# Kernel optimization log

Measured on AMD Instinct MI355X. Metric: run time of the kernel, lower is better.

## Reference

```python
import jax, jax.numpy as jnp
import numpy as np

N = 20000      # nodes
E = 320000     # edges (before self-loops)
C_IN, C_HID, C_OUT = 256, 256, 128
NEG_SLOPE = 0.2  # PyG GATConv default


def setup_inputs() -> dict:
    key = jax.random.key(0)
    ks = jax.random.split(key, 10)
    x = jax.random.normal(ks[0], (N, C_IN), dtype=jnp.float32)
    edge_index = jax.random.randint(ks[1], (2, E), 0, N, dtype=jnp.int64)

    def glorot(k, shape, fan):
        return jax.random.normal(k, shape, dtype=jnp.float32) / np.float32(np.sqrt(fan))

    W1 = glorot(ks[2], (C_IN, C_HID), C_IN)
    a_src1 = glorot(ks[3], (C_HID,), C_HID)
    a_dst1 = glorot(ks[4], (C_HID,), C_HID)
    b1 = jnp.zeros((C_HID,), jnp.float32)
    W2 = glorot(ks[5], (C_HID, C_OUT), C_HID)
    a_src2 = glorot(ks[6], (C_OUT,), C_OUT)
    a_dst2 = glorot(ks[7], (C_OUT,), C_OUT)
    b2 = jnp.zeros((C_OUT,), jnp.float32)
    return dict(x=x, edge_index=edge_index, W1=W1, a_src1=a_src1, a_dst1=a_dst1,
                b1=b1, W2=W2, a_src2=a_src2, a_dst2=a_dst2, b2=b2)


def gat_layer(x, src, dst, W, a_src, a_dst, b, n):
    # PyG GATConv (heads=1): linear proj, additive attention, softmax over
    # incoming edges per destination node, weighted aggregation + bias.
    h = x @ W                                   # [N, F]
    alpha_src = h @ a_src                       # [N]
    alpha_dst = h @ a_dst                       # [N]
    e = jax.nn.leaky_relu(alpha_src[src] + alpha_dst[dst], NEG_SLOPE)  # [E]
    m = jax.ops.segment_max(e, dst, num_segments=n)                    # stable softmax
    e = jnp.exp(e - m[dst])
    denom = jax.ops.segment_sum(e, dst, num_segments=n)                # [N]
    out = jax.ops.segment_sum(e[:, None] * h[src], dst, num_segments=n)  # [N, F]
    return out / denom[:, None] + b


def reference(x, edge_index, W1, a_src1, a_dst1, b1, W2, a_src2, a_dst2, b2):
    n = x.shape[0]
    # GATConv adds self-loops by default
    loops = jnp.arange(n, dtype=edge_index.dtype)
    ei = jnp.concatenate([edge_index, jnp.stack([loops, loops])], axis=1)
    src, dst = ei[0], ei[1]
    h = gat_layer(x, src, dst, W1, a_src1, a_dst1, b1, n)
    h = jax.nn.relu(h)  # Dropout is identity in eval mode
    return gat_layer(h, src, dst, W2, a_src2, a_dst2, b2, n)
```

## Files before the change

kernel.cpp:

```cpp
#include <hip/hip_runtime.h>
#include <math.h>

#define N_NODES 20000
#define N_EDGES 320000
#define C_IN  256
#define C_HID 256
#define C_OUT 128
#define NEG_SLOPE 0.2f
#define CAP   256
#define GEMM1_BLKS (N_NODES / 32)
#define SCAT_BLKS  ((N_EDGES + 255) / 256)
#define AGG_PAD 280

typedef __attribute__((ext_vector_type(8))) short bf16x8;
typedef __attribute__((ext_vector_type(4))) float f32x4;

__device__ __align__(16) unsigned short c_W1h[C_IN * C_HID], c_W1l[C_IN * C_HID];
__device__ __align__(16) unsigned short c_W2h[C_HID * C_OUT], c_W2l[C_HID * C_OUT];
__device__ float c_as1f[C_HID], c_ad1f[C_HID], c_b1f[C_HID];
__device__ float c_as2f[C_OUT], c_ad2f[C_OUT], c_b2f[C_OUT];
__device__ __align__(16) unsigned short g_h1b[(size_t)N_NODES * C_HID];
__device__ __align__(16) unsigned short g_h2b[(size_t)N_NODES * C_OUT];
__device__ float g_alps1[N_NODES], g_alpd1[N_NODES];
__device__ float g_alps2[N_NODES], g_alpd2[N_NODES];
__device__ int   g_cursor[N_NODES];
__device__ int   g_srcidx[(size_t)N_NODES * CAP];
__device__ int   g_is64;
__device__ int   g_isf32;

__device__ __forceinline__ float bf2f(unsigned short b){
  unsigned int u = ((unsigned int)b) << 16;
  return __builtin_bit_cast(float, u);
}
__device__ __forceinline__ unsigned short f2bf(float f){
  unsigned int u = __builtin_bit_cast(unsigned int, f);
  u += 0x7fffu + ((u >> 16) & 1u);
  return (unsigned short)(u >> 16);
}
__device__ __forceinline__ int clampi(int v){
  v = v < 0 ? 0 : v;
  return v >= N_NODES ? N_NODES - 1 : v;
}
__device__ __forceinline__ void edge_sd(const int* ei, int e, int& s, int& d){
  if (g_is64){ s = ei[2 * e]; d = ei[2 * (N_EDGES + e)]; }
  else       { s = ei[e];     d = ei[N_EDGES + e]; }
  s = clampi(s); d = clampi(d);
}

struct Ptrs { const void* p[8]; };

__device__ __forceinline__ int wpack(int k, int n, int Nc){
  return (((k >> 5) * (Nc / 16) + (n >> 4)) * 64 + (((k >> 3) & 3) * 16 + (n & 15))) * 8 + (k & 7);
}

#define PREP_Z  N_NODES
#define PREP_W1 (C_IN * C_HID)
#define PREP_W2 (C_HID * C_OUT)
#define PREP_T  (PREP_Z + PREP_W1 + PREP_W2 + 2 * C_HID + C_HID + 2 * C_OUT + C_OUT)

__global__ void prep_k(const unsigned int* __restrict__ xw,
                       const int* __restrict__ ei, Ptrs ps){
  __shared__ int s_isf32;
  if (threadIdx.x < 64){
    int lane = (int)threadIdx.x, cnt = 0;
    for (int j = lane; j < 256; j += 64){
      unsigned int e = (xw[j] >> 7) & 0xFFu;
      if (e >= 0x60u && e <= 0x8Fu) ++cnt;
    }
#pragma unroll
    for (int o = 32; o > 0; o >>= 1) cnt += __shfl_xor(cnt, o, 64);
    if (lane == 0) s_isf32 = (cnt < 200) ? 1 : 0;
  }
  __syncthreads();
  const int isf32 = s_isf32;

  if (blockIdx.x == 0 && threadIdx.x < 64){
    unsigned long long anybad = __ballot(ei[2 * (int)threadIdx.x + 1] != 0);
    if (threadIdx.x == 0){ g_isf32 = isf32; g_is64 = (anybad == 0ULL) ? 1 : 0; }
  }

  int tid = (int)(blockIdx.x * blockDim.x + threadIdx.x);
  if (tid < PREP_Z){
    g_cursor[tid] = 0;
    return;
  }
  int j = tid - PREP_Z;
  auto ld = [&](const void* p, int i) -> float {
    return isf32 ? ((const float*)p)[i] : bf2f(((const unsigned short*)p)[i]);
  };
  if (j < PREP_W1){
    float f = ld(ps.p[0], j);
    int k = j / C_HID, n = j % C_HID;
    int idx = wpack(k, n, C_HID);
    unsigned short h = f2bf(f);
    c_W1h[idx] = h; c_W1l[idx] = f2bf(f - bf2f(h));
    return;
  }
  j -= PREP_W1;
  if (j < PREP_W2){
    float f = ld(ps.p[4], j);
    int k = j / C_OUT, n = j % C_OUT;
    int idx = wpack(k, n, C_OUT);
    unsigned short h = f2bf(f);
    c_W2h[idx] = h; c_W2l[idx] = f2bf(f - bf2f(h));
    return;
  }
  j -= PREP_W2;
  if      (j <  256) c_as1f[j]        = ld(ps.p[1], j);
  else if (j <  512) c_ad1f[j - 256]  = ld(ps.p[2], j - 256);
  else if (j <  768) c_b1f [j - 512]  = ld(ps.p[3], j - 512);
  else if (j <  896) c_as2f[j - 768]  = ld(ps.p[5], j - 768);
  else if (j < 1024) c_ad2f[j - 896]  = ld(ps.p[6], j - 896);
  else if (j < 1152) c_b2f [j - 1024] = ld(ps.p[7], j - 1024);
}

__global__ __launch_bounds__(256) void gemm1_k(const void* __restrict__ xsrc,
                                               const int* __restrict__ ei){
  if (blockIdx.x >= GEMM1_BLKS){
    int e = (int)(blockIdx.x - GEMM1_BLKS) * 256 + (int)threadIdx.x;
    if (e < N_EDGES){
      int s, d;
      edge_sd(ei, e, s, d);
      int pos = atomicAdd(&g_cursor[d], 1);
      if (pos < CAP) g_srcidx[(size_t)d * CAP + pos] = s;
    }
    return;
  }

  __shared__ float s_ps[4][32], s_pd[4][32];

  const bool isf32 = (g_isf32 != 0);
  int wid  = (int)(threadIdx.x >> 6);
  int lane = (int)(threadIdx.x & 63);
  int kgrp = lane >> 4, cl = lane & 15;
  int mbase = blockIdx.x * 32;

  f32x4 acc[2][4];
#pragma unroll
  for (int m = 0; m < 2; ++m)
#pragma unroll
    for (int n = 0; n < 4; ++n) acc[m][n] = (f32x4){0.f, 0.f, 0.f, 0.f};

  for (int kt = 0; kt < 8; ++kt){
    int kbase = kt * 32 + kgrp * 8;
    bf16x8 ah[2], al[2];
    if (isf32){
      const float* Xf = (const float*)xsrc;
#pragma unroll
      for (int m = 0; m < 2; ++m){
        const float4* xp = (const float4*)(Xf + (size_t)(mbase + m * 16 + cl) * 256 + kbase);
        float4 v0 = xp[0], v1 = xp[1];
        float vals[8] = {v0.x, v0.y, v0.z, v0.w, v1.x, v1.y, v1.z, v1.w};
#pragma unroll
        for (int j = 0; j < 8; ++j){
          unsigned short h = f2bf(vals[j]);
          ah[m][j] = (short)h;
          al[m][j] = (short)f2bf(vals[j] - bf2f(h));
        }
      }
    } else {
      const unsigned short* Xb = (const unsigned short*)xsrc;
#pragma unroll
      for (int m = 0; m < 2; ++m){
        ah[m] = *(const bf16x8*)(Xb + (size_t)(mbase + m * 16 + cl) * 256 + kbase);
        al[m] = (bf16x8){0,0,0,0,0,0,0,0};
      }
    }
#pragma unroll
    for (int nn = 0; nn < 4; ++nn){
      int nt = wid * 4 + nn;
      size_t wi = ((size_t)(kt * 16 + nt) * 64 + lane) * 8;
      bf16x8 bh = *(const bf16x8*)(c_W1h + wi);
      bf16x8 bl = *(const bf16x8*)(c_W1l + wi);
#pragma unroll
      for (int m = 0; m < 2; ++m){
        acc[m][nn] = __builtin_amdgcn_mfma_f32_16x16x32_bf16(ah[m], bh, acc[m][nn], 0, 0, 0);
        acc[m][nn] = __builtin_amdgcn_mfma_f32_16x16x32_bf16(ah[m], bl, acc[m][nn], 0, 0, 0);
        acc[m][nn] = __builtin_amdgcn_mfma_f32_16x16x32_bf16(al[m], bh, acc[m][nn], 0, 0, 0);
      }
    }
  }

  float asv[4], adv[4];
#pragma unroll
  for (int nn = 0; nn < 4; ++nn){
    int col = (wid * 4 + nn) * 16 + cl;
    asv[nn] = c_as1f[col]; adv[nn] = c_ad1f[col];
  }
#pragma unroll
  for (int m = 0; m < 2; ++m){
#pragma unroll
    for (int i = 0; i < 4; ++i){
      int rl = m * 16 + kgrp * 4 + i;
      int row = mbase + rl;
      float ps = 0.f, pd = 0.f;
#pragma unroll
      for (int nn = 0; nn < 4; ++nn){
        int col = (wid * 4 + nn) * 16 + cl;
        float v = acc[m][nn][i];
        g_h1b[(size_t)row * C_HID + col] = f2bf(v);
        ps += v * asv[nn]; pd += v * adv[nn];
      }
      ps += __shfl_xor(ps, 1);  pd += __shfl_xor(pd, 1);
      ps += __shfl_xor(ps, 2);  pd += __shfl_xor(pd, 2);
      ps += __shfl_xor(ps, 4);  pd += __shfl_xor(pd, 4);
      ps += __shfl_xor(ps, 8);  pd += __shfl_xor(pd, 8);
      if (cl == 0){ s_ps[wid][rl] = ps; s_pd[wid][rl] = pd; }
    }
  }
  __syncthreads();
  if (threadIdx.x < 32){
    int r = (int)threadIdx.x;
    g_alps1[mbase + r] = s_ps[0][r] + s_ps[1][r] + s_ps[2][r] + s_ps[3][r];
    g_alpd1[mbase + r] = s_pd[0][r] + s_pd[1][r] + s_pd[2][r] + s_pd[3][r];
  }
}

#define ACC4(p, ww) { \
  a0 += (ww) * bf2f((unsigned short)((p).x & 0xFFFFu)); \
  a1 += (ww) * bf2f((unsigned short)((p).x >> 16)); \
  a2 += (ww) * bf2f((unsigned short)((p).y & 0xFFFFu)); \
  a3 += (ww) * bf2f((unsigned short)((p).y >> 16)); }

#define ACC2(p, ww) { \
  a0 += (ww) * bf2f((unsigned short)((p) & 0xFFFFu)); \
  a1 += (ww) * bf2f((unsigned short)((p) >> 16)); }

__global__ __launch_bounds__(256) void aggemm_k(){
  __shared__ __align__(16) unsigned short s_hi[16 * AGG_PAD];
  __shared__ __align__(16) unsigned short s_lo[16 * AGG_PAD];
  __shared__ float s_ps[4][16], s_pd[4][16];

  int lane = (int)(threadIdx.x & 63);
  int wid  = (int)(threadIdx.x >> 6);
  int nb   = blockIdx.x * 16;
  const uint2* H2 = (const uint2*)g_h1b;

  for (int q = 0; q < 4; ++q){
    int n = nb + wid * 4 + q;
    int len = g_cursor[n]; if (len > CAP) len = CAP;
    int i0 = n * CAP, i1 = i0 + len;
    float adn = g_alpd1[n];
    float dpart = 0.f;
    float a0 = 0.f, a1 = 0.f, a2 = 0.f, a3 = 0.f;

    {
      float es = g_alps1[n] + adn;
      es = (es > 0.f) ? es : NEG_SLOPE * es;
      float wself = __expf(es);
      if (lane == 0) dpart += wself;
      uint2 p = H2[(size_t)n * 64 + lane];
      ACC4(p, wself)
    }

    for (int base = i0; base < i1; base += 64){
      int nv = i1 - base; if (nv > 64) nv = 64;
      int sv = 0; float wv = 0.f;
      if (lane < nv){
        sv = g_srcidx[base + lane];
        float e = g_alps1[sv] + adn;
        e = (e > 0.f) ? e : NEG_SLOPE * e;
        wv = __expf(e);
      }
      dpart += wv;
      int j = 0;
      for (; j + 8 <= nv; j += 8){
        int s0 = __shfl(sv, j),     s1 = __shfl(sv, j + 1);
        int s2 = __shfl(sv, j + 2), s3 = __shfl(sv, j + 3);
        int s4 = __shfl(sv, j + 4), s5 = __shfl(sv, j + 5);
        int s6 = __shfl(sv, j + 6), s7 = __shfl(sv, j + 7);
        float w0 = __shfl(wv, j),     w1 = __shfl(wv, j + 1);
        float w2 = __shfl(wv, j + 2), w3 = __shfl(wv, j + 3);
        float w4 = __shfl(wv, j + 4), w5 = __shfl(wv, j + 5);
        float w6 = __shfl(wv, j + 6), w7 = __shfl(wv, j + 7);
        uint2 p0 = H2[(size_t)s0 * 64 + lane];
        uint2 p1 = H2[(size_t)s1 * 64 + lane];
        uint2 p2 = H2[(size_t)s2 * 64 + lane];
        uint2 p3 = H2[(size_t)s3 * 64 + lane];
        uint2 p4 = H2[(size_t)s4 * 64 + lane];
        uint2 p5 = H2[(size_t)s5 * 64 + lane];
        uint2 p6 = H2[(size_t)s6 * 64 + lane];
        uint2 p7 = H2[(size_t)s7 * 64 + lane];
        ACC4(p0, w0) ACC4(p1, w1) ACC4(p2, w2) ACC4(p3, w3)
        ACC4(p4, w4) ACC4(p5, w5) ACC4(p6, w6) ACC4(p7, w7)
      }
      for (; j + 4 <= nv; j += 4){
        int s0 = __shfl(sv, j),     s1 = __shfl(sv, j + 1);
        int s2 = __shfl(sv, j + 2), s3 = __shfl(sv, j + 3);
        float w0 = __shfl(wv, j),     w1 = __shfl(wv, j + 1);
        float w2 = __shfl(wv, j + 2), w3 = __shfl(wv, j + 3);
        uint2 p0 = H2[(size_t)s0 * 64 + lane];
        uint2 p1 = H2[(size_t)s1 * 64 + lane];
        uint2 p2 = H2[(size_t)s2 * 64 + lane];
        uint2 p3 = H2[(size_t)s3 * 64 + lane];
        ACC4(p0, w0) ACC4(p1, w1) ACC4(p2, w2) ACC4(p3, w3)
      }
      for (; j < nv; ++j){
        int s = __shfl(sv, j);
        float w = __shfl(wv, j);
        uint2 p = H2[(size_t)s * 64 + lane];
        ACC4(p, w)
      }
    }

    float den = dpart;
#pragma unroll
    for (int o = 32; o > 0; o >>= 1) den += __shfl_xor(den, o, 64);
    float inv = 1.f / den;

    float o0 = a0 * inv + c_b1f[4 * lane];
    float o1 = a1 * inv + c_b1f[4 * lane + 1];
    float o2 = a2 * inv + c_b1f[4 * lane + 2];
    float o3 = a3 * inv + c_b1f[4 * lane + 3];
    o0 = fmaxf(o0, 0.f); o1 = fmaxf(o1, 0.f);
    o2 = fmaxf(o2, 0.f); o3 = fmaxf(o3, 0.f);
    unsigned short h0 = f2bf(o0), h1 = f2bf(o1), h2 = f2bf(o2), h3 = f2bf(o3);
    uint2 ph, pl;
    ph.x = (unsigned)h0 | ((unsigned)h1 << 16);
    ph.y = (unsigned)h2 | ((unsigned)h3 << 16);
    pl.x = (unsigned)f2bf(o0 - bf2f(h0)) | ((unsigned)f2bf(o1 - bf2f(h1)) << 16);
    pl.y = (unsigned)f2bf(o2 - bf2f(h2)) | ((unsigned)f2bf(o3 - bf2f(h3)) << 16);
    int r = wid * 4 + q;
    *(uint2*)&s_hi[r * AGG_PAD + 4 * lane] = ph;
    *(uint2*)&s_lo[r * AGG_PAD + 4 * lane] = pl;
  }
  __syncthreads();

  int kgrp = lane >> 4, cl = lane & 15;
  f32x4 acc[2];
  acc[0] = (f32x4){0.f, 0.f, 0.f, 0.f};
  acc[1] = (f32x4){0.f, 0.f, 0.f, 0.f};
  for (int kt = 0; kt < 8; ++kt){
    int rb = cl * AGG_PAD + kt * 32 + kgrp * 8;
    bf16x8 ah = *(const bf16x8*)&s_hi[rb];
    bf16x8 al = *(const bf16x8*)&s_lo[rb];
#pragma unroll
    for (int nn = 0; nn < 2; ++nn){
      int nt = wid * 2 + nn;
      size_t wi = ((size_t)(kt * 8 + nt) * 64 + lane) * 8;
      bf16x8 bh = *(const bf16x8*)(c_W2h + wi);
      bf16x8 bl = *(const bf16x8*)(c_W2l + wi);
      acc[nn] = __builtin_amdgcn_mfma_f32_16x16x32_bf16(ah, bh, acc[nn], 0, 0, 0);
      acc[nn] = __builtin_amdgcn_mfma_f32_16x16x32_bf16(ah, bl, acc[nn], 0, 0, 0);
      acc[nn] = __builtin_amdgcn_mfma_f32_16x16x32_bf16(al, bh, acc[nn], 0, 0, 0);
    }
  }

  float asv[2], adv[2];
#pragma unroll
  for (int nn = 0; nn < 2; ++nn){
    int col = (wid * 2 + nn) * 16 + cl;
    asv[nn] = c_as2f[col]; adv[nn] = c_ad2f[col];
  }
#pragma unroll
  for (int i = 0; i < 4; ++i){
    int row = nb + kgrp * 4 + i;
    float ps = 0.f, pd = 0.f;
#pragma unroll
    for (int nn = 0; nn < 2; ++nn){
      int col = (wid * 2 + nn) * 16 + cl;
      float v = acc[nn][i];
      g_h2b[(size_t)row * C_OUT + col] = f2bf(v);
      ps += v * asv[nn]; pd += v * adv[nn];
    }
    ps += __shfl_xor(ps, 1);  pd += __shfl_xor(pd, 1);
    ps += __shfl_xor(ps, 2);  pd += __shfl_xor(pd, 2);
    ps += __shfl_xor(ps, 4);  pd += __shfl_xor(pd, 4);
    ps += __shfl_xor(ps, 8);  pd += __shfl_xor(pd, 8);
    if (cl == 0){ s_ps[wid][kgrp * 4 + i] = ps; s_pd[wid][kgrp * 4 + i] = pd; }
  }
  __syncthreads();
  if (threadIdx.x < 16){
    int r = (int)threadIdx.x;
    g_alps2[nb + r] = s_ps[0][r] + s_ps[1][r] + s_ps[2][r] + s_ps[3][r];
    g_alpd2[nb + r] = s_pd[0][r] + s_pd[1][r] + s_pd[2][r] + s_pd[3][r];
  }
}

__global__ __launch_bounds__(256) void agg2_k(float* OUT){
  int lane = (int)(threadIdx.x & 63);
  int n = blockIdx.x * 4 + (int)(threadIdx.x >> 6);
  int len = g_cursor[n]; if (len > CAP) len = CAP;
  int i0 = n * CAP, i1 = i0 + len;
  float adn = g_alpd2[n];
  float dpart = 0.f;
  float a0 = 0.f, a1 = 0.f;
  const unsigned int* H1 = (const unsigned int*)g_h2b;

  {
    float es = g_alps2[n] + adn;
    es = (es > 0.f) ? es : NEG_SLOPE * es;
    float wself = __expf(es);
    if (lane == 0) dpart += wself;
    unsigned int p = H1[(size_t)n * 64 + lane];
    ACC2(p, wself)
  }

  for (int base = i0; base < i1; base += 64){
    int nv = i1 - base; if (nv > 64) nv = 64;
    int sv = 0; float wv = 0.f;
    if (lane < nv){
      sv = g_srcidx[base + lane];
      float e = g_alps2[sv] + adn;
      e = (e > 0.f) ? e : NEG_SLOPE * e;
      wv = __expf(e);
    }
    dpart += wv;
    int j = 0;
    for (; j + 8 <= nv; j += 8){
      int s0 = __shfl(sv, j),     s1 = __shfl(sv, j + 1);
      int s2 = __shfl(sv, j + 2), s3 = __shfl(sv, j + 3);
      int s4 = __shfl(sv, j + 4), s5 = __shfl(sv, j + 5);
      int s6 = __shfl(sv, j + 6), s7 = __shfl(sv, j + 7);
      float w0 = __shfl(wv, j),     w1 = __shfl(wv, j + 1);
      float w2 = __shfl(wv, j + 2), w3 = __shfl(wv, j + 3);
      float w4 = __shfl(wv, j + 4), w5 = __shfl(wv, j + 5);
      float w6 = __shfl(wv, j + 6), w7 = __shfl(wv, j + 7);
      unsigned int p0 = H1[(size_t)s0 * 64 + lane];
      unsigned int p1 = H1[(size_t)s1 * 64 + lane];
      unsigned int p2 = H1[(size_t)s2 * 64 + lane];
      unsigned int p3 = H1[(size_t)s3 * 64 + lane];
      unsigned int p4 = H1[(size_t)s4 * 64 + lane];
      unsigned int p5 = H1[(size_t)s5 * 64 + lane];
      unsigned int p6 = H1[(size_t)s6 * 64 + lane];
      unsigned int p7 = H1[(size_t)s7 * 64 + lane];
      ACC2(p0, w0) ACC2(p1, w1) ACC2(p2, w2) ACC2(p3, w3)
      ACC2(p4, w4) ACC2(p5, w5) ACC2(p6, w6) ACC2(p7, w7)
    }
    for (; j + 4 <= nv; j += 4){
      int s0 = __shfl(sv, j),     s1 = __shfl(sv, j + 1);
      int s2 = __shfl(sv, j + 2), s3 = __shfl(sv, j + 3);
      float w0 = __shfl(wv, j),     w1 = __shfl(wv, j + 1);
      float w2 = __shfl(wv, j + 2), w3 = __shfl(wv, j + 3);
      unsigned int p0 = H1[(size_t)s0 * 64 + lane];
      unsigned int p1 = H1[(size_t)s1 * 64 + lane];
      unsigned int p2 = H1[(size_t)s2 * 64 + lane];
      unsigned int p3 = H1[(size_t)s3 * 64 + lane];
      ACC2(p0, w0) ACC2(p1, w1) ACC2(p2, w2) ACC2(p3, w3)
    }
    for (; j < nv; ++j){
      int s = __shfl(sv, j);
      float w = __shfl(wv, j);
      unsigned int p = H1[(size_t)s * 64 + lane];
      ACC2(p, w)
    }
  }

  float den = dpart;
#pragma unroll
  for (int o = 32; o > 0; o >>= 1) den += __shfl_xor(den, o, 64);
  float inv = 1.f / den;

  float2 o;
  o.x = a0 * inv + c_b2f[2 * lane];
  o.y = a1 * inv + c_b2f[2 * lane + 1];
  ((float2*)OUT)[(size_t)n * 64 + lane] = o;
}

extern "C" void kernel_launch(void* const* d_in, const int* in_sizes, int n_in,
                              void* d_out, int out_size, void* d_ws, size_t ws_size,
                              hipStream_t stream){
  (void)in_sizes; (void)n_in; (void)out_size; (void)d_ws; (void)ws_size;
  const void* x  = d_in[0];
  const int*  ei = (const int*)d_in[1];
  float* out = (float*)d_out;

  Ptrs ps;
  ps.p[0] = d_in[2]; ps.p[1] = d_in[3]; ps.p[2] = d_in[4]; ps.p[3] = d_in[5];
  ps.p[4] = d_in[6]; ps.p[5] = d_in[7]; ps.p[6] = d_in[8]; ps.p[7] = d_in[9];

  prep_k<<<(PREP_T + 255) / 256, 256, 0, stream>>>((const unsigned int*)x, ei, ps);

  gemm1_k<<<GEMM1_BLKS + SCAT_BLKS, 256, 0, stream>>>(x, ei);

  aggemm_k<<<N_NODES / 16, 256, 0, stream>>>();

  agg2_k<<<N_NODES / 4, 256, 0, stream>>>(out);
}
```

Baseline: 164.6 us.

## Fuse all GAT stages into one cooperative persistent kernel with grid syncs

Merges the prep, GEMM1-plus-scatter, aggregate-plus-GEMM2 and final aggregation kernels into a single cooperative kernel. Stages are separated by grid-wide syncs, and within each stage work tiles are handed out through global atomic counters. The aim is to remove the separate kernel launches and the idle tail between stages. In exchange it adds grid-sync cost, one atomic per tile, and occupancy limits from `launch_bounds(256,4)`, with a fallback to the old multi-kernel path if the cooperative launch fails.

```diff
diff --git a/kernel.cpp b/kernel.cpp
--- a/kernel.cpp
+++ b/kernel.cpp
@@ -1,5 +1,8 @@
 #include <hip/hip_runtime.h>
+#include <hip/hip_cooperative_groups.h>
 #include <math.h>
+
+namespace cg = cooperative_groups;
 
 #define N_NODES 20000
 #define N_EDGES 320000
@@ -10,6 +13,8 @@
 #define CAP   256
 #define GEMM1_BLKS (N_NODES / 32)
 #define SCAT_BLKS  ((N_EDGES + 255) / 256)
+#define AGGEMM_BLKS (N_NODES / 16)
+#define AGG2_BLKS  (N_NODES / 4)
 #define AGG_PAD 280
 
 typedef __attribute__((ext_vector_type(8))) short bf16x8;
@@ -27,6 +32,7 @@
 __device__ int   g_srcidx[(size_t)N_NODES * CAP];
 __device__ int   g_is64;
 __device__ int   g_isf32;
+__device__ int   g_q1, g_q2, g_q3;
 
 __device__ __forceinline__ float bf2f(unsigned short b){
   unsigned int u = ((unsigned int)b) << 16;
@@ -41,22 +47,442 @@
   v = v < 0 ? 0 : v;
   return v >= N_NODES ? N_NODES - 1 : v;
 }
+
+struct Ptrs { const void* p[8]; };
+
+__device__ __forceinline__ int wpack(int k, int n, int Nc){
+  return (((k >> 5) * (Nc / 16) + (n >> 4)) * 64 + (((k >> 3) & 3) * 16 + (n & 15))) * 8 + (k & 7);
+}
+
+#define PREP_Z  N_NODES
+#define PREP_W1 (C_IN * C_HID)
+#define PREP_W2 (C_HID * C_OUT)
+#define PREP_T  (PREP_Z + PREP_W1 + PREP_W2 + 2 * C_HID + C_HID + 2 * C_OUT + C_OUT)
+
+#define ACC4(p, ww) { \
+  a0 += (ww) * bf2f((unsigned short)((p).x & 0xFFFFu)); \
+  a1 += (ww) * bf2f((unsigned short)((p).x >> 16)); \
+  a2 += (ww) * bf2f((unsigned short)((p).y & 0xFFFFu)); \
+  a3 += (ww) * bf2f((unsigned short)((p).y >> 16)); }
+
+#define ACC2(p, ww) { \
+  a0 += (ww) * bf2f((unsigned short)((p) & 0xFFFFu)); \
+  a1 += (ww) * bf2f((unsigned short)((p) >> 16)); }
+
+__global__ __launch_bounds__(256, 4) void fused_k(const unsigned int* __restrict__ xw,
+                                                  const int* __restrict__ ei,
+                                                  float* __restrict__ OUT,
+                                                  Ptrs ps){
+  __shared__ __align__(16) unsigned short s_hi[16 * AGG_PAD];
+  __shared__ __align__(16) unsigned short s_lo[16 * AGG_PAD];
+  __shared__ float s_ps[4][32], s_pd[4][32];
+  __shared__ int s_flags, s_vb;
+
+  const int tidx = (int)threadIdx.x;
+  const int lane = tidx & 63;
+  const int wid  = tidx >> 6;
+
+  if (tidx < 64){
+    int cnt = 0;
+    for (int j = lane; j < 256; j += 64){
+      unsigned int e = (xw[j] >> 7) & 0xFFu;
+      if (e >= 0x60u && e <= 0x8Fu) ++cnt;
+    }
+#pragma unroll
+    for (int o = 32; o > 0; o >>= 1) cnt += __shfl_xor(cnt, o, 64);
+    unsigned long long anybad = __ballot(ei[2 * lane + 1] != 0);
+    if (lane == 0) s_flags = ((cnt < 200) ? 1 : 0) | ((anybad == 0ULL) ? 2 : 0);
+  }
+  if (blockIdx.x == 0 && tidx == 0){ g_q1 = 0; g_q2 = 0; g_q3 = 0; }
+  __syncthreads();
+  const bool isf32 = (s_flags & 1) != 0;
+  const bool is64  = (s_flags & 2) != 0;
+
+  const int total = (int)(gridDim.x * blockDim.x);
+  auto ld = [&](const void* p, int i) -> float {
+    return isf32 ? ((const float*)p)[i] : bf2f(((const unsigned short*)p)[i]);
+  };
+  for (int t = (int)(blockIdx.x * blockDim.x) + tidx; t < PREP_T; t += total){
+    if (t < PREP_Z){ g_cursor[t] = 0; continue; }
+    int j = t - PREP_Z;
+    if (j < PREP_W1){
+      float f = ld(ps.p[0], j);
+      int k = j / C_HID, n = j % C_HID;
+      int idx = wpack(k, n, C_HID);
+      unsigned short h = f2bf(f);
+      c_W1h[idx] = h; c_W1l[idx] = f2bf(f - bf2f(h));
+      continue;
+    }
+    j -= PREP_W1;
+    if (j < PREP_W2){
+      float f = ld(ps.p[4], j);
+      int k = j / C_OUT, n = j % C_OUT;
+      int idx = wpack(k, n, C_OUT);
+      unsigned short h = f2bf(f);
+      c_W2h[idx] = h; c_W2l[idx] = f2bf(f - bf2f(h));
+      continue;
+    }
+    j -= PREP_W2;
+    if      (j <  256) c_as1f[j]        = ld(ps.p[1], j);
+    else if (j <  512) c_ad1f[j - 256]  = ld(ps.p[2], j - 256);
+    else if (j <  768) c_b1f [j - 512]  = ld(ps.p[3], j - 512);
+    else if (j <  896) c_as2f[j - 768]  = ld(ps.p[5], j - 768);
+    else if (j < 1024) c_ad2f[j - 896]  = ld(ps.p[6], j - 896);
+    else if (j < 1152) c_b2f [j - 1024] = ld(ps.p[7], j - 1024);
+  }
+
+  __threadfence();
+  cg::this_grid().sync();
+
+  for (;;){
+    __syncthreads();
+    if (tidx == 0) s_vb = atomicAdd(&g_q1, 1);
+    __syncthreads();
+    const int vb = s_vb;
+    if (vb >= GEMM1_BLKS + SCAT_BLKS) break;
+
+    if (vb >= GEMM1_BLKS){
+      int e = (vb - GEMM1_BLKS) * 256 + tidx;
+      if (e < N_EDGES){
+        int s, d;
+        if (is64){ s = ei[2 * e]; d = ei[2 * (N_EDGES + e)]; }
+        else     { s = ei[e];     d = ei[N_EDGES + e]; }
+        s = clampi(s); d = clampi(d);
+        int pos = atomicAdd(&g_cursor[d], 1);
+        if (pos < CAP) g_srcidx[(size_t)d * CAP + pos] = s;
+      }
+      continue;
+    }
+
+    int kgrp = lane >> 4, cl = lane & 15;
+    int mbase = vb * 32;
+    f32x4 acc[2][4];
+#pragma unroll
+    for (int m = 0; m < 2; ++m)
+#pragma unroll
+      for (int n = 0; n < 4; ++n) acc[m][n] = (f32x4){0.f, 0.f, 0.f, 0.f};
+
+    for (int kt = 0; kt < 8; ++kt){
+      int kbase = kt * 32 + kgrp * 8;
+      bf16x8 ah[2], al[2];
+      if (isf32){
+        const float* Xf = (const float*)xw;
+#pragma unroll
+        for (int m = 0; m < 2; ++m){
+          const float4* xp = (const float4*)(Xf + (size_t)(mbase + m * 16 + cl) * 256 + kbase);
+          float4 v0 = xp[0], v1 = xp[1];
+          float vals[8] = {v0.x, v0.y, v0.z, v0.w, v1.x, v1.y, v1.z, v1.w};
+#pragma unroll
+          for (int j = 0; j < 8; ++j){
+            unsigned short h = f2bf(vals[j]);
+            ah[m][j] = (short)h;
+            al[m][j] = (short)f2bf(vals[j] - bf2f(h));
+          }
+        }
+      } else {
+        const unsigned short* Xb = (const unsigned short*)xw;
+#pragma unroll
+        for (int m = 0; m < 2; ++m){
+          ah[m] = *(const bf16x8*)(Xb + (size_t)(mbase + m * 16 + cl) * 256 + kbase);
+          al[m] = (bf16x8){0,0,0,0,0,0,0,0};
+        }
+      }
+#pragma unroll
+      for (int nn = 0; nn < 4; ++nn){
+        int nt = wid * 4 + nn;
+        size_t wi = ((size_t)(kt * 16 + nt) * 64 + lane) * 8;
+        bf16x8 bh = *(const bf16x8*)(c_W1h + wi);
+        bf16x8 bl = *(const bf16x8*)(c_W1l + wi);
+#pragma unroll
+        for (int m = 0; m < 2; ++m){
+          acc[m][nn] = __builtin_amdgcn_mfma_f32_16x16x32_bf16(ah[m], bh, acc[m][nn], 0, 0, 0);
+          acc[m][nn] = __builtin_amdgcn_mfma_f32_16x16x32_bf16(ah[m], bl, acc[m][nn], 0, 0, 0);
+          acc[m][nn] = __builtin_amdgcn_mfma_f32_16x16x32_bf16(al[m], bh, acc[m][nn], 0, 0, 0);
+        }
+      }
+    }
+
+    float asv[4], adv[4];
+#pragma unroll
+    for (int nn = 0; nn < 4; ++nn){
+      int col = (wid * 4 + nn) * 16 + cl;
+      asv[nn] = c_as1f[col]; adv[nn] = c_ad1f[col];
+    }
+#pragma unroll
+    for (int m = 0; m < 2; ++m){
+#pragma unroll
+      for (int i = 0; i < 4; ++i){
+        int rl = m * 16 + kgrp * 4 + i;
+        int row = mbase + rl;
+        float psum = 0.f, pdum = 0.f;
+#pragma unroll
+        for (int nn = 0; nn < 4; ++nn){
+          int col = (wid * 4 + nn) * 16 + cl;
+          float v = acc[m][nn][i];
+          g_h1b[(size_t)row * C_HID + col] = f2bf(v);
+          psum += v * asv[nn]; pdum += v * adv[nn];
+        }
+        psum += __shfl_xor(psum, 1);  pdum += __shfl_xor(pdum, 1);
+        psum += __shfl_xor(psum, 2);  pdum += __shfl_xor(pdum, 2);
+        psum += __shfl_xor(psum, 4);  pdum += __shfl_xor(pdum, 4);
+        psum += __shfl_xor(psum, 8);  pdum += __shfl_xor(pdum, 8);
+        if (cl == 0){ s_ps[wid][rl] = psum; s_pd[wid][rl] = pdum; }
+      }
+    }
+    __syncthreads();
+    if (tidx < 32){
+      int r = tidx;
+      g_alps1[mbase + r] = s_ps[0][r] + s_ps[1][r] + s_ps[2][r] + s_ps[3][r];
+      g_alpd1[mbase + r] = s_pd[0][r] + s_pd[1][r] + s_pd[2][r] + s_pd[3][r];
+    }
+  }
+
+  __threadfence();
+  cg::this_grid().sync();
+
+  for (;;){
+    __syncthreads();
+    if (tidx == 0) s_vb = atomicAdd(&g_q2, 1);
+    __syncthreads();
+    const int vb = s_vb;
+    if (vb >= AGGEMM_BLKS) break;
+    const int nb = vb * 16;
+    const uint2* H2 = (const uint2*)g_h1b;
+
+    for (int q = 0; q < 4; ++q){
+      int n = nb + wid * 4 + q;
+      int len = g_cursor[n]; if (len > CAP) len = CAP;
+      int i0 = n * CAP, i1 = i0 + len;
+      float adn = g_alpd1[n];
+      float dpart = 0.f;
+      float a0 = 0.f, a1 = 0.f, a2 = 0.f, a3 = 0.f;
+
+      {
+        float es = g_alps1[n] + adn;
+        es = (es > 0.f) ? es : NEG_SLOPE * es;
+        float wself = __expf(es);
+        if (lane == 0) dpart += wself;
+        uint2 p = H2[(size_t)n * 64 + lane];
+        ACC4(p, wself)
+      }
+
+      for (int base = i0; base < i1; base += 64){
+        int nv = i1 - base; if (nv > 64) nv = 64;
+        int sv = 0; float wv = 0.f;
+        if (lane < nv){
+          sv = g_srcidx[base + lane];
+          float e = g_alps1[sv] + adn;
+          e = (e > 0.f) ? e : NEG_SLOPE * e;
+          wv = __expf(e);
+        }
+        dpart += wv;
+        int j = 0;
+        for (; j + 8 <= nv; j += 8){
+          int t0 = __shfl(sv, j),     t1 = __shfl(sv, j + 1);
+          int t2 = __shfl(sv, j + 2), t3 = __shfl(sv, j + 3);
+          int t4 = __shfl(sv, j + 4), t5 = __shfl(sv, j + 5);
+          int t6 = __shfl(sv, j + 6), t7 = __shfl(sv, j + 7);
+          float w0 = __shfl(wv, j),     w1 = __shfl(wv, j + 1);
+          float w2 = __shfl(wv, j + 2), w3 = __shfl(wv, j + 3);
+          float w4 = __shfl(wv, j + 4), w5 = __shfl(wv, j + 5);
+          float w6 = __shfl(wv, j + 6), w7 = __shfl(wv, j + 7);
+          uint2 p0 = H2[(size_t)t0 * 64 + lane];
+          uint2 p1 = H2[(size_t)t1 * 64 + lane];
+          uint2 p2 = H2[(size_t)t2 * 64 + lane];
+          uint2 p3 = H2[(size_t)t3 * 64 + lane];
+          uint2 p4 = H2[(size_t)t4 * 64 + lane];
+          uint2 p5 = H2[(size_t)t5 * 64 + lane];
+          uint2 p6 = H2[(size_t)t6 * 64 + lane];
+          uint2 p7 = H2[(size_t)t7 * 64 + lane];
+          ACC4(p0, w0) ACC4(p1, w1) ACC4(p2, w2) ACC4(p3, w3)
+          ACC4(p4, w4) ACC4(p5, w5) ACC4(p6, w6) ACC4(p7, w7)
+        }
+        for (; j + 4 <= nv; j += 4){
+          int t0 = __shfl(sv, j),     t1 = __shfl(sv, j + 1);
+          int t2 = __shfl(sv, j + 2), t3 = __shfl(sv, j + 3);
+          float w0 = __shfl(wv, j),     w1 = __shfl(wv, j + 1);
+          float w2 = __shfl(wv, j + 2), w3 = __shfl(wv, j + 3);
+          uint2 p0 = H2[(size_t)t0 * 64 + lane];
+          uint2 p1 = H2[(size_t)t1 * 64 + lane];
+          uint2 p2 = H2[(size_t)t2 * 64 + lane];
+          uint2 p3 = H2[(size_t)t3 * 64 + lane];
+          ACC4(p0, w0) ACC4(p1, w1) ACC4(p2, w2) ACC4(p3, w3)
+        }
+        for (; j < nv; ++j){
+          int t = __shfl(sv, j);
+          float w = __shfl(wv, j);
+          uint2 p = H2[(size_t)t * 64 + lane];
+          ACC4(p, w)
+        }
+      }
+
+      float den = dpart;
+#pragma unroll
+      for (int o = 32; o > 0; o >>= 1) den += __shfl_xor(den, o, 64);
+      float inv = 1.f / den;
+
+      float o0 = a0 * inv + c_b1f[4 * lane];
+      float o1 = a1 * inv + c_b1f[4 * lane + 1];
+      float o2 = a2 * inv + c_b1f[4 * lane + 2];
+      float o3 = a3 * inv + c_b1f[4 * lane + 3];
+      o0 = fmaxf(o0, 0.f); o1 = fmaxf(o1, 0.f);
+      o2 = fmaxf(o2, 0.f); o3 = fmaxf(o3, 0.f);
+      unsigned short h0 = f2bf(o0), h1 = f2bf(o1), h2 = f2bf(o2), h3 = f2bf(o3);
+      uint2 ph, pl;
+      ph.x = (unsigned)h0 | ((unsigned)h1 << 16);
+      ph.y = (unsigned)h2 | ((unsigned)h3 << 16);
+      pl.x = (unsigned)f2bf(o0 - bf2f(h0)) | ((unsigned)f2bf(o1 - bf2f(h1)) << 16);
+      pl.y = (unsigned)f2bf(o2 - bf2f(h2)) | ((unsigned)f2bf(o3 - bf2f(h3)) << 16);
+      int r = wid * 4 + q;
+      *(uint2*)&s_hi[r * AGG_PAD + 4 * lane] = ph;
+      *(uint2*)&s_lo[r * AGG_PAD + 4 * lane] = pl;
+    }
+    __syncthreads();
+
+    int kgrp = lane >> 4, cl = lane & 15;
+    f32x4 acc2[2];
+    acc2[0] = (f32x4){0.f, 0.f, 0.f, 0.f};
+    acc2[1] = (f32x4){0.f, 0.f, 0.f, 0.f};
+    for (int kt = 0; kt < 8; ++kt){
+      int rb = cl * AGG_PAD + kt * 32 + kgrp * 8;
+      bf16x8 ah = *(const bf16x8*)&s_hi[rb];
+      bf16x8 al = *(const bf16x8*)&s_lo[rb];
+#pragma unroll
+      for (int nn = 0; nn < 2; ++nn){
+        int nt = wid * 2 + nn;
+        size_t wi = ((size_t)(kt * 8 + nt) * 64 + lane) * 8;
+        bf16x8 bh = *(const bf16x8*)(c_W2h + wi);
+        bf16x8 bl = *(const bf16x8*)(c_W2l + wi);
+        acc2[nn] = __builtin_amdgcn_mfma_f32_16x16x32_bf16(ah, bh, acc2[nn], 0, 0, 0);
+        acc2[nn] = __builtin_amdgcn_mfma_f32_16x16x32_bf16(ah, bl, acc2[nn], 0, 0, 0);
+        acc2[nn] = __builtin_amdgcn_mfma_f32_16x16x32_bf16(al, bh, acc2[nn], 0, 0, 0);
+      }
+    }
+
+    float asv[2], adv[2];
+#pragma unroll
+    for (int nn = 0; nn < 2; ++nn){
+      int col = (wid * 2 + nn) * 16 + cl;
+      asv[nn] = c_as2f[col]; adv[nn] = c_ad2f[col];
+    }
+#pragma unroll
+    for (int i = 0; i < 4; ++i){
+      int row = nb + kgrp * 4 + i;
+      float psum = 0.f, pdum = 0.f;
+#pragma unroll
+      for (int nn = 0; nn < 2; ++nn){
+        int col = (wid * 2 + nn) * 16 + cl;
+        float v = acc2[nn][i];
+        g_h2b[(size_t)row * C_OUT + col] = f2bf(v);
+        psum += v * asv[nn]; pdum += v * adv[nn];
+      }
+      psum += __shfl_xor(psum, 1);  pdum += __shfl_xor(pdum, 1);
+      psum += __shfl_xor(psum, 2);  pdum += __shfl_xor(pdum, 2);
+      psum += __shfl_xor(psum, 4);  pdum += __shfl_xor(pdum, 4);
+      psum += __shfl_xor(psum, 8);  pdum += __shfl_xor(pdum, 8);
+      if (cl == 0){ s_ps[wid][kgrp * 4 + i] = psum; s_pd[wid][kgrp * 4 + i] = pdum; }
+    }
+    __syncthreads();
+    if (tidx < 16){
+      int r = tidx;
+      g_alps2[nb + r] = s_ps[0][r] + s_ps[1][r] + s_ps[2][r] + s_ps[3][r];
+      g_alpd2[nb + r] = s_pd[0][r] + s_pd[1][r] + s_pd[2][r] + s_pd[3][r];
+    }
+  }
+
+  __threadfence();
+  cg::this_grid().sync();
+
+  const unsigned int* H1 = (const unsigned int*)g_h2b;
+  for (;;){
+    __syncthreads();
+    if (tidx == 0) s_vb = atomicAdd(&g_q3, 1);
+    __syncthreads();
+    const int vb = s_vb;
+    if (vb >= AGG2_BLKS) break;
+    int n = vb * 4 + wid;
+    int len = g_cursor[n]; if (len > CAP) len = CAP;
+    int i0 = n * CAP, i1 = i0 + len;
+    float adn = g_alpd2[n];
+    float dpart = 0.f;
+    float a0 = 0.f, a1 = 0.f;
+
+    {
+      float es = g_alps2[n] + adn;
+      es = (es > 0.f) ? es : NEG_SLOPE * es;
+      float wself = __expf(es);
+      if (lane == 0) dpart += wself;
+      unsigned int p = H1[(size_t)n * 64 + lane];
+      ACC2(p, wself)
+    }
+
+    for (int base = i0; base < i1; base += 64){
+      int nv = i1 - base; if (nv > 64) nv = 64;
+      int sv = 0; float wv = 0.f;
+      if (lane < nv){
+        sv = g_srcidx[base + lane];
+        float e = g_alps2[sv] + adn;
+        e = (e > 0.f) ? e : NEG_SLOPE * e;
+        wv = __expf(e);
+      }
+      dpart += wv;
+      int j = 0;
+      for (; j + 8 <= nv; j += 8){
+        int t0 = __shfl(sv, j),     t1 = __shfl(sv, j + 1);
+        int t2 = __shfl(sv, j + 2), t3 = __shfl(sv, j + 3);
+        int t4 = __shfl(sv, j + 4), t5 = __shfl(sv, j + 5);
+        int t6 = __shfl(sv, j + 6), t7 = __shfl(sv, j + 7);
+        float w0 = __shfl(wv, j),     w1 = __shfl(wv, j + 1);
+        float w2 = __shfl(wv, j + 2), w3 = __shfl(wv, j + 3);
+        float w4 = __shfl(wv, j + 4), w5 = __shfl(wv, j + 5);
+        float w6 = __shfl(wv, j + 6), w7 = __shfl(wv, j + 7);
+        unsigned int p0 = H1[(size_t)t0 * 64 + lane];
+        unsigned int p1 = H1[(size_t)t1 * 64 + lane];
+        unsigned int p2 = H1[(size_t)t2 * 64 + lane];
+        unsigned int p3 = H1[(size_t)t3 * 64 + lane];
+        unsigned int p4 = H1[(size_t)t4 * 64 + lane];
+        unsigned int p5 = H1[(size_t)t5 * 64 + lane];
+        unsigned int p6 = H1[(size_t)t6 * 64 + lane];
+        unsigned int p7 = H1[(size_t)t7 * 64 + lane];
+        ACC2(p0, w0) ACC2(p1, w1) ACC2(p2, w2) ACC2(p3, w3)
+        ACC2(p4, w4) ACC2(p5, w5) ACC2(p6, w6) ACC2(p7, w7)
+      }
+      for (; j + 4 <= nv; j += 4){
+        int t0 = __shfl(sv, j),     t1 = __shfl(sv, j + 1);
+        int t2 = __shfl(sv, j + 2), t3 = __shfl(sv, j + 3);
+        float w0 = __shfl(wv, j),     w1 = __shfl(wv, j + 1);
+        float w2 = __shfl(wv, j + 2), w3 = __shfl(wv, j + 3);
+        unsigned int p0 = H1[(size_t)t0 * 64 + lane];
+        unsigned int p1 = H1[(size_t)t1 * 64 + lane];
+        unsigned int p2 = H1[(size_t)t2 * 64 + lane];
+        unsigned int p3 = H1[(size_t)t3 * 64 + lane];
+        ACC2(p0, w0) ACC2(p1, w1) ACC2(p2, w2) ACC2(p3, w3)
+      }
+      for (; j < nv; ++j){
+        int t = __shfl(sv, j);
+        float w = __shfl(wv, j);
+        unsigned int p = H1[(size_t)t * 64 + lane];
+        ACC2(p, w)
+      }
+    }
+
+    float den = dpart;
+#pragma unroll
+    for (int o = 32; o > 0; o >>= 1) den += __shfl_xor(den, o, 64);
+    float inv = 1.f / den;
+
+    float2 o;
+    o.x = a0 * inv + c_b2f[2 * lane];
+    o.y = a1 * inv + c_b2f[2 * lane + 1];
+    ((float2*)OUT)[(size_t)n * 64 + lane] = o;
+  }
+}
+
 __device__ __forceinline__ void edge_sd(const int* ei, int e, int& s, int& d){
   if (g_is64){ s = ei[2 * e]; d = ei[2 * (N_EDGES + e)]; }
   else       { s = ei[e];     d = ei[N_EDGES + e]; }
   s = clampi(s); d = clampi(d);
 }
-
-struct Ptrs { const void* p[8]; };
-
-__device__ __forceinline__ int wpack(int k, int n, int Nc){
-  return (((k >> 5) * (Nc / 16) + (n >> 4)) * 64 + (((k >> 3) & 3) * 16 + (n & 15))) * 8 + (k & 7);
-}
-
-#define PREP_Z  N_NODES
-#define PREP_W1 (C_IN * C_HID)
-#define PREP_W2 (C_HID * C_OUT)
-#define PREP_T  (PREP_Z + PREP_W1 + PREP_W2 + 2 * C_HID + C_HID + 2 * C_OUT + C_OUT)
 
 __global__ void prep_k(const unsigned int* __restrict__ xw,
                        const int* __restrict__ ei, Ptrs ps){
@@ -80,10 +506,7 @@
   }
 
   int tid = (int)(blockIdx.x * blockDim.x + threadIdx.x);
-  if (tid < PREP_Z){
-    g_cursor[tid] = 0;
-    return;
-  }
+  if (tid < PREP_Z){ g_cursor[tid] = 0; return; }
   int j = tid - PREP_Z;
   auto ld = [&](const void* p, int i) -> float {
     return isf32 ? ((const float*)p)[i] : bf2f(((const unsigned short*)p)[i]);
@@ -128,7 +551,6 @@
   }
 
   __shared__ float s_ps[4][32], s_pd[4][32];
-
   const bool isf32 = (g_isf32 != 0);
   int wid  = (int)(threadIdx.x >> 6);
   int lane = (int)(threadIdx.x & 63);
@@ -215,16 +637,6 @@
     g_alpd1[mbase + r] = s_pd[0][r] + s_pd[1][r] + s_pd[2][r] + s_pd[3][r];
   }
 }
-
-#define ACC4(p, ww) { \
-  a0 += (ww) * bf2f((unsigned short)((p).x & 0xFFFFu)); \
-  a1 += (ww) * bf2f((unsigned short)((p).x >> 16)); \
-  a2 += (ww) * bf2f((unsigned short)((p).y & 0xFFFFu)); \
-  a3 += (ww) * bf2f((unsigned short)((p).y >> 16)); }
-
-#define ACC2(p, ww) { \
-  a0 += (ww) * bf2f((unsigned short)((p) & 0xFFFFu)); \
-  a1 += (ww) * bf2f((unsigned short)((p) >> 16)); }
 
 __global__ __launch_bounds__(256) void aggemm_k(){
   __shared__ __align__(16) unsigned short s_hi[16 * AGG_PAD];
@@ -469,11 +881,26 @@
   ps.p[0] = d_in[2]; ps.p[1] = d_in[3]; ps.p[2] = d_in[4]; ps.p[3] = d_in[5];
   ps.p[4] = d_in[6]; ps.p[5] = d_in[7]; ps.p[6] = d_in[8]; ps.p[7] = d_in[9];
 
+  static int coop_grid = -1;
+  if (coop_grid < 0){
+    int nb = 0;
+    if (hipOccupancyMaxActiveBlocksPerMultiprocessor(&nb, fused_k, 256, 0) != hipSuccess) nb = 0;
+    int g = nb * 256;
+    if (g > 2048) g = 2048;
+    coop_grid = (nb > 0) ? g : 0;
+  }
+  if (coop_grid > 0){
+    const unsigned int* xw = (const unsigned int*)x;
+    void* args[4] = { (void*)&xw, (void*)&ei, (void*)&out, (void*)&ps };
+    hipError_t err = hipLaunchCooperativeKernel((const void*)fused_k,
+                                                dim3((unsigned)coop_grid), dim3(256),
+                                                args, 0, stream);
+    if (err == hipSuccess) return;
+    coop_grid = 0;
+  }
+
   prep_k<<<(PREP_T + 255) / 256, 256, 0, stream>>>((const unsigned int*)x, ei, ps);
-
   gemm1_k<<<GEMM1_BLKS + SCAT_BLKS, 256, 0, stream>>>(x, ei);
-
-  aggemm_k<<<N_NODES / 16, 256, 0, stream>>>();
-
-  agg2_k<<<N_NODES / 4, 256, 0, stream>>>(out);
-}
+  aggemm_k<<<AGGEMM_BLKS, 256, 0, stream>>>();
+  agg2_k<<<AGG2_BLKS, 256, 0, stream>>>(out);
+}
```

Result: slower. 622.1 us (+277.9%).
